# Kernel optimization log

Measured on AMD Instinct MI355X. Metric: run time of the kernel, lower is better.

The kernel has to match this reference:

```python
import jax, jax.numpy as jnp
import numpy as np

T, B, I, H = 2048, 512, 10, 20  # seq_len, batch, input_size, hidden_size
G = 4 * H  # gate dim, PyTorch order: i, f, g, o


def _lstm_scan(x, w_ih, w_hh, b_ih, b_hh):
    # x: [T, B, I]; w_ih: [4H, I]; w_hh: [4H, H]; biases: [4H]
    # Precompute input projection for all timesteps (one big GEMM).
    x_proj = jnp.einsum('tbi,gi->tbg', x, w_ih) + b_ih + b_hh  # [T, B, 4H]

    def step(carry, xg):
        h, c = carry
        gates = xg + h @ w_hh.T  # [B, 4H]
        i, f, g, o = jnp.split(gates, 4, axis=-1)
        i = jax.nn.sigmoid(i)
        f = jax.nn.sigmoid(f)
        g = jnp.tanh(g)
        o = jax.nn.sigmoid(o)
        c = f * c + i * g
        h = o * jnp.tanh(c)
        return (h, c), h

    h0 = jnp.zeros((x.shape[1], H), x.dtype)
    c0 = jnp.zeros((x.shape[1], H), x.dtype)
    _, hs = jax.lax.scan(step, (h0, c0), x_proj)
    return hs  # [T, B, H]


def setup_inputs() -> dict:
    key = jax.random.key(0)
    ks = jax.random.split(key, 9)
    s_ih = 1.0 / np.sqrt(H)
    inp = {
        'x': jax.random.normal(ks[0], (T, B, I, 1), dtype=jnp.float32),
        'w_ih_f': jax.random.uniform(ks[1], (G, I), jnp.float32, -s_ih, s_ih),
        'w_hh_f': jax.random.uniform(ks[2], (G, H), jnp.float32, -s_ih, s_ih),
        'b_ih_f': jax.random.uniform(ks[3], (G,), jnp.float32, -s_ih, s_ih),
        'b_hh_f': jax.random.uniform(ks[4], (G,), jnp.float32, -s_ih, s_ih),
        'w_ih_r': jax.random.uniform(ks[5], (G, I), jnp.float32, -s_ih, s_ih),
        'w_hh_r': jax.random.uniform(ks[6], (G, H), jnp.float32, -s_ih, s_ih),
        'b_ih_r': jax.random.uniform(ks[7], (G,), jnp.float32, -s_ih, s_ih),
        'b_hh_r': jax.random.uniform(ks[8], (G,), jnp.float32, -s_ih, s_ih),
    }
    return inp


def reference(x, w_ih_f, w_hh_f, b_ih_f, b_hh_f, w_ih_r, w_hh_r, b_ih_r, b_hh_r):
    xs = jnp.squeeze(x, -1)  # [T, B, I]
    out_f = _lstm_scan(xs, w_ih_f, w_hh_f, b_ih_f, b_hh_f)            # forward dir
    out_r = _lstm_scan(xs[::-1], w_ih_r, w_hh_r, b_ih_r, b_hh_r)[::-1]  # reverse dir
    return jnp.concatenate([out_f, out_r], axis=-1)  # [T, B, 2H]
```

## Files before the change

### kernel.cpp

```cpp
#include <hip/hip_runtime.h>

typedef float f2 __attribute__((ext_vector_type(2)));
typedef float f4 __attribute__((ext_vector_type(4)));

#define TT 2048
#define BB 512
#define II 10
#define HH 20
#define CH 16
#define RS 32
#define NCHUNK (TT / CH)

#define LOG2E 1.44269504088896340736f

__device__ __forceinline__ float fexp2(float x) {
#if __has_builtin(__builtin_amdgcn_exp2f)
    return __builtin_amdgcn_exp2f(x);
#else
    return exp2f(x);
#endif
}

__global__ __launch_bounds__(128) void lstm_bidir(
    const float* __restrict__ x,
    const float* __restrict__ w_ih_f, const float* __restrict__ w_hh_f,
    const float* __restrict__ b_ih_f, const float* __restrict__ b_hh_f,
    const float* __restrict__ w_ih_r, const float* __restrict__ w_hh_r,
    const float* __restrict__ b_ih_r, const float* __restrict__ b_hh_r,
    float* __restrict__ out)
{
    const int tid  = threadIdx.x;
    const int wid  = tid >> 6;
    const int lane = tid & 63;
    const int blk  = blockIdx.x;
    const int dir  = blk >> 9;
    const int s    = blk & 511;

    const float* __restrict__ w_ih = dir ? w_ih_r : w_ih_f;
    const float* __restrict__ w_hh = dir ? w_hh_r : w_hh_f;
    const float* __restrict__ b_ih = dir ? b_ih_r : b_ih_f;
    const float* __restrict__ b_hh = dir ? b_hh_r : b_hh_f;

    const bool valid = (lane < HH);
    const int  j     = valid ? lane : (HH - 1);

    const int t0    = dir ? (TT - 1) : 0;
    const int xstep = dir ? -(BB * II) : (BB * II);
    const int ostep = dir ? -(BB * 2 * HH) : (BB * 2 * HH);
    const int xbase = (t0 * BB + s) * II;

    const float gsc[4] = { -LOG2E, -LOG2E, -2.0f * LOG2E, -LOG2E };

    __shared__ f4    ring[RS][HH];
    __shared__ float hstage[CH * 64];

    if (wid == 1) {
        f2 wih[4][5];
        float bs[4];
#pragma unroll
        for (int g = 0; g < 4; ++g) {
            const int r = g * HH + j;
#pragma unroll
            for (int k = 0; k < 5; ++k) {
                f2 w = *(const f2*)(w_ih + r * II + 2 * k);
                wih[g][k] = w * gsc[g];
            }
            bs[g] = (b_ih[r] + b_hh[r]) * gsc[g];
        }

        auto produce8 = [&](int base) {
            f2 xb[8][5];
#pragma unroll
            for (int i = 0; i < 8; ++i) {
                int u = base + i; if (u > TT - 1) u = TT - 1;
                const float* px = x + (xbase + u * xstep);
#pragma unroll
                for (int k = 0; k < 5; ++k) xb[i][k] = *(const f2*)(px + 2 * k);
            }
#pragma unroll
            for (int i = 0; i < 8; ++i) {
                const int u = base + i;
                if (u < TT) {
                    f4 xp;
#pragma unroll
                    for (int g = 0; g < 4; ++g) {
                        f2 p = {bs[g], 0.f};
#pragma unroll
                        for (int k = 0; k < 5; ++k) p += wih[g][k] * xb[i][k];
                        xp[g] = p[0] + p[1];
                    }
                    if (valid) ring[u & (RS - 1)][j] = xp;
                }
            }
        };

        produce8(0);
        produce8(8);
        for (int chunk = 0; chunk < NCHUNK; ++chunk) {
            __syncthreads();
            const int base = (chunk + 1) * CH;
            produce8(base);
            produce8(base + 8);
        }
    } else {
        __builtin_amdgcn_s_setprio(1);

        f2 whh[4][10];
#pragma unroll
        for (int g = 0; g < 4; ++g) {
            const int r = g * HH + j;
#pragma unroll
            for (int k = 0; k < 10; ++k) {
                f2 w = *(const f2*)(w_hh + r * HH + 2 * k);
                whh[g][k] = w * gsc[g];
            }
        }

        const int obase = (t0 * BB + s) * (2 * HH) + dir * HH;
        int offd[5], lds_d[5];
#pragma unroll
        for (int q = 0; q < 5; ++q) {
            const int idx = q * 64 + lane;
            const int td  = idx / HH;
            const int jd  = idx - td * HH;
            offd[q]  = obase + td * ostep + jd;
            lds_d[q] = td * 64 + jd;
        }

        f4 hb[5];
#pragma unroll
        for (int k = 0; k < 5; ++k) hb[k] = f4{0.f, 0.f, 0.f, 0.f};

        float c = 0.0f, h = 0.0f;
        int t = 0;

        for (int chunk = 0; chunk < NCHUNK; ++chunk) {
            __syncthreads();
            f4 xp = ring[t & (RS - 1)][j];
#pragma unroll
            for (int i = 0; i < CH; ++i, ++t) {
                f2 a0[4], a1[4];
#pragma unroll
                for (int g = 0; g < 4; ++g) { a0[g] = f2{0.f, 0.f}; a1[g] = f2{0.f, 0.f}; }
#pragma unroll
                for (int k = 0; k < 5; ++k) {
                    const f4 hv = hb[k];
                    f2 lo; lo[0] = hv[0]; lo[1] = hv[1];
                    f2 hi; hi[0] = hv[2]; hi[1] = hv[3];
#pragma unroll
                    for (int g = 0; g < 4; ++g) {
                        a0[g] += whh[g][2 * k]     * lo;
                        a1[g] += whh[g][2 * k + 1] * hi;
                    }
                }
                float u[4];
#pragma unroll
                for (int g = 0; g < 4; ++g) {
                    const f2 a = a0[g] + a1[g];
                    u[g] = (xp[g] + a[0]) + a[1];
                }

                const float ig = __builtin_amdgcn_rcpf(1.0f + fexp2(u[0]));
                const float fg = __builtin_amdgcn_rcpf(1.0f + fexp2(u[1]));
                const float sg = __builtin_amdgcn_rcpf(1.0f + fexp2(u[2]));
                const float og = __builtin_amdgcn_rcpf(1.0f + fexp2(u[3]));
                const float i2 = ig + ig;
                const float o2 = og + og;

                const float m = __builtin_fmaf(i2, sg, -ig);
                c = __builtin_fmaf(fg, c, m);
                const float sc_ = __builtin_amdgcn_rcpf(
                                    1.0f + fexp2(c * (-2.0f * LOG2E)));
                h = __builtin_fmaf(o2, sc_, -og);

                hstage[i * 64 + lane] = h;
                __builtin_amdgcn_wave_barrier();

#pragma unroll
                for (int k = 0; k < 5; ++k)
                    hb[k] = *(const f4*)&hstage[i * 64 + 4 * k];

                if (i < CH - 1) xp = ring[(t + 1) & (RS - 1)][j];
            }

#pragma unroll
            for (int q = 0; q < 5; ++q) {
                const float v = hstage[lds_d[q]];
                out[offd[q]] = v;
                offd[q] += CH * ostep;
            }
        }
    }
}

extern "C" void kernel_launch(void* const* d_in, const int* in_sizes, int n_in,
                              void* d_out, int out_size, void* d_ws, size_t ws_size,
                              hipStream_t stream) {
    const float* xp     = (const float*)d_in[0];
    const float* w_ih_f = (const float*)d_in[1];
    const float* w_hh_f = (const float*)d_in[2];
    const float* b_ih_f = (const float*)d_in[3];
    const float* b_hh_f = (const float*)d_in[4];
    const float* w_ih_r = (const float*)d_in[5];
    const float* w_hh_r = (const float*)d_in[6];
    const float* b_ih_r = (const float*)d_in[7];
    const float* b_hh_r = (const float*)d_in[8];
    float* outp = (float*)d_out;

    hipLaunchKernelGGL(lstm_bidir, dim3(1024), dim3(128), 0, stream,
                       xp, w_ih_f, w_hh_f, b_ih_f, b_hh_f,
                       w_ih_r, w_hh_r, b_ih_r, b_hh_r, outp);
}
```

Before: 525.0 us.

## Pack forward and reverse directions into the two half-waves of one block

Each block now handles one batch element for both directions: lanes 0-31 run the forward LSTM and lanes 32-63 run the reverse one, so the grid is halved from 1024 to 512 blocks. Before, 44 of the 64 lanes in each wave were idle; now both halves of the wave do useful work on the serial recurrence. The cost is per-lane direction selection for pointers and strides, and twice as many output-store slots per chunk.

New measurement: 506.7 us. -3.5%, faster.

```diff
diff --git a/kernel.cpp b/kernel.cpp
--- a/kernel.cpp
+++ b/kernel.cpp
@@ -32,26 +32,26 @@
     const int tid  = threadIdx.x;
     const int wid  = tid >> 6;
     const int lane = tid & 63;
-    const int blk  = blockIdx.x;
-    const int dir  = blk >> 9;
-    const int s    = blk & 511;
-
-    const float* __restrict__ w_ih = dir ? w_ih_r : w_ih_f;
-    const float* __restrict__ w_hh = dir ? w_hh_r : w_hh_f;
-    const float* __restrict__ b_ih = dir ? b_ih_r : b_ih_f;
-    const float* __restrict__ b_hh = dir ? b_hh_r : b_hh_f;
-
-    const bool valid = (lane < HH);
-    const int  j     = valid ? lane : (HH - 1);
-
-    const int t0    = dir ? (TT - 1) : 0;
-    const int xstep = dir ? -(BB * II) : (BB * II);
-    const int ostep = dir ? -(BB * 2 * HH) : (BB * 2 * HH);
+    const int s    = blockIdx.x;
+
+    const int  dirh = lane >> 5;
+    const int  hl   = lane & 31;
+    const bool valid = (hl < HH);
+    const int  j     = valid ? hl : (HH - 1);
+
+    const float* __restrict__ w_ih = dirh ? w_ih_r : w_ih_f;
+    const float* __restrict__ w_hh = dirh ? w_hh_r : w_hh_f;
+    const float* __restrict__ b_ih = dirh ? b_ih_r : b_ih_f;
+    const float* __restrict__ b_hh = dirh ? b_hh_r : b_hh_f;
+
+    const int t0    = dirh ? (TT - 1) : 0;
+    const int xstep = dirh ? -(BB * II) : (BB * II);
+    const int ostep = dirh ? -(BB * 2 * HH) : (BB * 2 * HH);
     const int xbase = (t0 * BB + s) * II;
 
     const float gsc[4] = { -LOG2E, -LOG2E, -2.0f * LOG2E, -LOG2E };
 
-    __shared__ f4    ring[RS][HH];
+    __shared__ f4    ring[RS][64];
     __shared__ float hstage[CH * 64];
 
     if (wid == 1) {
@@ -89,7 +89,7 @@
                         for (int k = 0; k < 5; ++k) p += wih[g][k] * xb[i][k];
                         xp[g] = p[0] + p[1];
                     }
-                    if (valid) ring[u & (RS - 1)][j] = xp;
+                    ring[u & (RS - 1)][lane] = xp;
                 }
             }
         };
@@ -116,16 +116,18 @@
             }
         }
 
-        const int obase = (t0 * BB + s) * (2 * HH) + dir * HH;
-        int offd[5], lds_d[5];
-#pragma unroll
-        for (int q = 0; q < 5; ++q) {
-            const int idx = q * 64 + lane;
+        const int obase = (t0 * BB + s) * (2 * HH) + dirh * HH;
+        int offd[10], lds_d[10];
+#pragma unroll
+        for (int q = 0; q < 10; ++q) {
+            const int idx = q * 32 + hl;
             const int td  = idx / HH;
             const int jd  = idx - td * HH;
             offd[q]  = obase + td * ostep + jd;
-            lds_d[q] = td * 64 + jd;
-        }
+            lds_d[q] = td * 64 + dirh * 32 + jd;
+        }
+
+        const int hboff = dirh * 32;
 
         f4 hb[5];
 #pragma unroll
@@ -136,7 +138,7 @@
 
         for (int chunk = 0; chunk < NCHUNK; ++chunk) {
             __syncthreads();
-            f4 xp = ring[t & (RS - 1)][j];
+            f4 xp = ring[t & (RS - 1)][lane];
 #pragma unroll
             for (int i = 0; i < CH; ++i, ++t) {
                 f2 a0[4], a1[4];
@@ -178,13 +180,13 @@
 
 #pragma unroll
                 for (int k = 0; k < 5; ++k)
-                    hb[k] = *(const f4*)&hstage[i * 64 + 4 * k];
-
-                if (i < CH - 1) xp = ring[(t + 1) & (RS - 1)][j];
-            }
-
-#pragma unroll
-            for (int q = 0; q < 5; ++q) {
+                    hb[k] = *(const f4*)&hstage[i * 64 + hboff + 4 * k];
+
+                if (i < CH - 1) xp = ring[(t + 1) & (RS - 1)][lane];
+            }
+
+#pragma unroll
+            for (int q = 0; q < 10; ++q) {
                 const float v = hstage[lds_d[q]];
                 out[offd[q]] = v;
                 offd[q] += CH * ostep;
@@ -207,7 +209,7 @@
     const float* b_hh_r = (const float*)d_in[8];
     float* outp = (float*)d_out;
 
-    hipLaunchKernelGGL(lstm_bidir, dim3(1024), dim3(128), 0, stream,
+    hipLaunchKernelGGL(lstm_bidir, dim3(512), dim3(128), 0, stream,
                        xp, w_ih_f, w_hh_f, b_ih_f, b_hh_f,
                        w_ih_r, w_hh_r, b_ih_r, b_hh_r, outp);
 }
```

## Merge producer wave into recurrence wave with register-pipelined input projection

Applied to the files above, without the earlier changes.

Removes the separate producer wavefront and its LDS ring plus block-wide barriers. A single 64-lane wave now computes the input projection inline, with x loads software-pipelined three steps ahead in registers. The gate math is also reworked so that sigmoid(i)*tanh(g) and sigmoid(o)*tanh(c) each need one reciprocal instead of two. The cost is more per-step work on the serial critical path and higher register pressure in the single wave.

Result: slower. 646.8 us (+23.2%).

```diff
diff --git a/kernel.cpp b/kernel.cpp
--- a/kernel.cpp
+++ b/kernel.cpp
@@ -8,7 +8,6 @@
 #define II 10
 #define HH 20
 #define CH 16
-#define RS 32
 #define NCHUNK (TT / CH)
 
 #define LOG2E 1.44269504088896340736f
@@ -21,7 +20,7 @@
 #endif
 }
 
-__global__ __launch_bounds__(128) void lstm_bidir(
+__global__ __launch_bounds__(64) void lstm_bidir(
     const float* __restrict__ x,
     const float* __restrict__ w_ih_f, const float* __restrict__ w_hh_f,
     const float* __restrict__ b_ih_f, const float* __restrict__ b_hh_f,
@@ -29,9 +28,7 @@
     const float* __restrict__ b_ih_r, const float* __restrict__ b_hh_r,
     float* __restrict__ out)
 {
-    const int tid  = threadIdx.x;
-    const int wid  = tid >> 6;
-    const int lane = tid & 63;
+    const int lane = threadIdx.x;
     const int blk  = blockIdx.x;
     const int dir  = blk >> 9;
     const int s    = blk & 511;
@@ -44,151 +41,136 @@
     const bool valid = (lane < HH);
     const int  j     = valid ? lane : (HH - 1);
 
+    const float gsc[4] = { -LOG2E, -LOG2E, -2.0f * LOG2E, -LOG2E };
+
+    f2 whh[4][10], wih[4][5];
+    float bs[4];
+#pragma unroll
+    for (int g = 0; g < 4; ++g) {
+        const int r = g * HH + j;
+#pragma unroll
+        for (int k = 0; k < 10; ++k) {
+            f2 w = *(const f2*)(w_hh + r * HH + 2 * k);
+            whh[g][k] = w * gsc[g];
+        }
+#pragma unroll
+        for (int k = 0; k < 5; ++k) {
+            f2 w = *(const f2*)(w_ih + r * II + 2 * k);
+            wih[g][k] = w * gsc[g];
+        }
+        bs[g] = (b_ih[r] + b_hh[r]) * gsc[g];
+    }
+
+    __shared__ float hstage[CH][HH];
+
     const int t0    = dir ? (TT - 1) : 0;
     const int xstep = dir ? -(BB * II) : (BB * II);
     const int ostep = dir ? -(BB * 2 * HH) : (BB * 2 * HH);
     const int xbase = (t0 * BB + s) * II;
 
-    const float gsc[4] = { -LOG2E, -LOG2E, -2.0f * LOG2E, -LOG2E };
+    const int obase = (t0 * BB + s) * (2 * HH) + dir * HH;
+    int offd[5], tdq[5], jdq[5];
+#pragma unroll
+    for (int q = 0; q < 5; ++q) {
+        const int idx = q * 64 + lane;
+        tdq[q] = idx / HH;
+        jdq[q] = idx - tdq[q] * HH;
+        offd[q] = obase + tdq[q] * ostep + jdq[q];
+    }
 
-    __shared__ f4    ring[RS][HH];
-    __shared__ float hstage[CH * 64];
-
-    if (wid == 1) {
-        f2 wih[4][5];
-        float bs[4];
+    f2 xb1[5], xb2[5], xb3[5];
+    float xp[4];
+    {
+        f2 x0[5];
+#pragma unroll
+        for (int k = 0; k < 5; ++k) x0[k]  = *(const f2*)(x + xbase + 2 * k);
+#pragma unroll
+        for (int k = 0; k < 5; ++k) xb1[k] = *(const f2*)(x + xbase + xstep + 2 * k);
+#pragma unroll
+        for (int k = 0; k < 5; ++k) xb2[k] = *(const f2*)(x + xbase + 2 * xstep + 2 * k);
+#pragma unroll
+        for (int k = 0; k < 5; ++k) xb3[k] = *(const f2*)(x + xbase + 3 * xstep + 2 * k);
 #pragma unroll
         for (int g = 0; g < 4; ++g) {
-            const int r = g * HH + j;
+            f2 p = {bs[g], 0.f};
+#pragma unroll
+            for (int k = 0; k < 5; ++k) p += wih[g][k] * x0[k];
+            xp[g] = p[0] + p[1];
+        }
+    }
+    int xoff4 = xbase + 4 * xstep;
+
+    f4 hb[5];
+#pragma unroll
+    for (int k = 0; k < 5; ++k) hb[k] = f4{0.f, 0.f, 0.f, 0.f};
+
+    float c = 0.0f, h = 0.0f;
+    int t = 0;
+
+    for (int chunk = 0; chunk < NCHUNK; ++chunk) {
+#pragma unroll
+        for (int i = 0; i < CH; ++i, ++t) {
+            f2 a0[4], a1[4];
+#pragma unroll
+            for (int g = 0; g < 4; ++g) { a0[g] = f2{xp[g], 0.f}; a1[g] = f2{0.f, 0.f}; }
 #pragma unroll
             for (int k = 0; k < 5; ++k) {
-                f2 w = *(const f2*)(w_ih + r * II + 2 * k);
-                wih[g][k] = w * gsc[g];
-            }
-            bs[g] = (b_ih[r] + b_hh[r]) * gsc[g];
-        }
-
-        auto produce8 = [&](int base) {
-            f2 xb[8][5];
+                const f4 hv = hb[k];
+                f2 lo; lo[0] = hv[0]; lo[1] = hv[1];
+                f2 hi; hi[0] = hv[2]; hi[1] = hv[3];
 #pragma unroll
-            for (int i = 0; i < 8; ++i) {
-                int u = base + i; if (u > TT - 1) u = TT - 1;
-                const float* px = x + (xbase + u * xstep);
-#pragma unroll
-                for (int k = 0; k < 5; ++k) xb[i][k] = *(const f2*)(px + 2 * k);
-            }
-#pragma unroll
-            for (int i = 0; i < 8; ++i) {
-                const int u = base + i;
-                if (u < TT) {
-                    f4 xp;
-#pragma unroll
-                    for (int g = 0; g < 4; ++g) {
-                        f2 p = {bs[g], 0.f};
-#pragma unroll
-                        for (int k = 0; k < 5; ++k) p += wih[g][k] * xb[i][k];
-                        xp[g] = p[0] + p[1];
-                    }
-                    if (valid) ring[u & (RS - 1)][j] = xp;
+                for (int g = 0; g < 4; ++g) {
+                    a0[g] += whh[g][2 * k]     * lo;
+                    a1[g] += whh[g][2 * k + 1] * hi;
                 }
             }
-        };
+            float u[4];
+#pragma unroll
+            for (int g = 0; g < 4; ++g) {
+                const f2 a = a0[g] + a1[g];
+                u[g] = a[0] + a[1];
+            }
 
-        produce8(0);
-        produce8(8);
-        for (int chunk = 0; chunk < NCHUNK; ++chunk) {
-            __syncthreads();
-            const int base = (chunk + 1) * CH;
-            produce8(base);
-            produce8(base + 8);
-        }
-    } else {
-        __builtin_amdgcn_s_setprio(1);
+            const float ei = fexp2(u[0]);
+            const float ef = fexp2(u[1]);
+            const float eg = fexp2(u[2]);
+            const float eo = fexp2(u[3]);
+            const float fg = __builtin_amdgcn_rcpf(1.0f + ef);
+            const float m  = (1.0f - eg) *
+                __builtin_amdgcn_rcpf((1.0f + ei) * (1.0f + eg));
+            c = __builtin_fmaf(fg, c, m);
+            const float ec = fexp2(c * (-2.0f * LOG2E));
+            h = (1.0f - ec) *
+                __builtin_amdgcn_rcpf((1.0f + eo) * (1.0f + ec));
 
-        f2 whh[4][10];
+            if (valid) hstage[i][lane] = h;
+            __builtin_amdgcn_wave_barrier();
 #pragma unroll
-        for (int g = 0; g < 4; ++g) {
-            const int r = g * HH + j;
+            for (int k = 0; k < 5; ++k)
+                hb[k] = *(const f4*)&hstage[i][4 * k];
+
+            f2 xb4[5];
 #pragma unroll
-            for (int k = 0; k < 10; ++k) {
-                f2 w = *(const f2*)(w_hh + r * HH + 2 * k);
-                whh[g][k] = w * gsc[g];
-            }
-        }
-
-        const int obase = (t0 * BB + s) * (2 * HH) + dir * HH;
-        int offd[5], lds_d[5];
-#pragma unroll
-        for (int q = 0; q < 5; ++q) {
-            const int idx = q * 64 + lane;
-            const int td  = idx / HH;
-            const int jd  = idx - td * HH;
-            offd[q]  = obase + td * ostep + jd;
-            lds_d[q] = td * 64 + jd;
-        }
-
-        f4 hb[5];
-#pragma unroll
-        for (int k = 0; k < 5; ++k) hb[k] = f4{0.f, 0.f, 0.f, 0.f};
-
-        float c = 0.0f, h = 0.0f;
-        int t = 0;
-
-        for (int chunk = 0; chunk < NCHUNK; ++chunk) {
-            __syncthreads();
-            f4 xp = ring[t & (RS - 1)][j];
-#pragma unroll
-            for (int i = 0; i < CH; ++i, ++t) {
-                f2 a0[4], a1[4];
-#pragma unroll
-                for (int g = 0; g < 4; ++g) { a0[g] = f2{0.f, 0.f}; a1[g] = f2{0.f, 0.f}; }
-#pragma unroll
-                for (int k = 0; k < 5; ++k) {
-                    const f4 hv = hb[k];
-                    f2 lo; lo[0] = hv[0]; lo[1] = hv[1];
-                    f2 hi; hi[0] = hv[2]; hi[1] = hv[3];
-#pragma unroll
-                    for (int g = 0; g < 4; ++g) {
-                        a0[g] += whh[g][2 * k]     * lo;
-                        a1[g] += whh[g][2 * k + 1] * hi;
-                    }
-                }
-                float u[4];
-#pragma unroll
-                for (int g = 0; g < 4; ++g) {
-                    const f2 a = a0[g] + a1[g];
-                    u[g] = (xp[g] + a[0]) + a[1];
-                }
-
-                const float ig = __builtin_amdgcn_rcpf(1.0f + fexp2(u[0]));
-                const float fg = __builtin_amdgcn_rcpf(1.0f + fexp2(u[1]));
-                const float sg = __builtin_amdgcn_rcpf(1.0f + fexp2(u[2]));
-                const float og = __builtin_amdgcn_rcpf(1.0f + fexp2(u[3]));
-                const float i2 = ig + ig;
-                const float o2 = og + og;
-
-                const float m = __builtin_fmaf(i2, sg, -ig);
-                c = __builtin_fmaf(fg, c, m);
-                const float sc_ = __builtin_amdgcn_rcpf(
-                                    1.0f + fexp2(c * (-2.0f * LOG2E)));
-                h = __builtin_fmaf(o2, sc_, -og);
-
-                hstage[i * 64 + lane] = h;
-                __builtin_amdgcn_wave_barrier();
+            for (int k = 0; k < 5; ++k) xb4[k] = *(const f2*)(x + xoff4 + 2 * k);
+            xoff4 += (t < TT - 5) ? xstep : 0;
 
 #pragma unroll
-                for (int k = 0; k < 5; ++k)
-                    hb[k] = *(const f4*)&hstage[i * 64 + 4 * k];
-
-                if (i < CH - 1) xp = ring[(t + 1) & (RS - 1)][j];
+            for (int g = 0; g < 4; ++g) {
+                f2 p = {bs[g], 0.f};
+#pragma unroll
+                for (int k = 0; k < 5; ++k) p += wih[g][k] * xb1[k];
+                xp[g] = p[0] + p[1];
             }
 
 #pragma unroll
-            for (int q = 0; q < 5; ++q) {
-                const float v = hstage[lds_d[q]];
-                out[offd[q]] = v;
-                offd[q] += CH * ostep;
-            }
+            for (int k = 0; k < 5; ++k) { xb1[k] = xb2[k]; xb2[k] = xb3[k]; xb3[k] = xb4[k]; }
+        }
+
+        __builtin_amdgcn_wave_barrier();
+#pragma unroll
+        for (int q = 0; q < 5; ++q) {
+            out[offd[q]] = hstage[tdq[q]][jdq[q]];
+            offd[q] += CH * ostep;
         }
     }
 }
@@ -207,7 +189,7 @@
     const float* b_hh_r = (const float*)d_in[8];
     float* outp = (float*)d_out;
 
-    hipLaunchKernelGGL(lstm_bidir, dim3(1024), dim3(128), 0, stream,
+    hipLaunchKernelGGL(lstm_bidir, dim3(1024), dim3(64), 0, stream,
                        xp, w_ih_f, w_hh_f, b_ih_f, b_hh_f,
                        w_ih_r, w_hh_r, b_ih_r, b_hh_r, outp);
 }
```
